# Performance work log

Measured on AMD Instinct MI355X. Metric: run time of the kernel, lower is better.

Reference implementation:

```python
import jax, jax.numpy as jnp
import numpy as np

EMBED = 1024
HEADS = 16
HEAD_DIM = EMBED // HEADS


def setup_inputs() -> dict:
    key = jax.random.key(0)
    ks = jax.random.split(key, 10)
    B, S = 2, 2048
    x = jax.random.normal(ks[0], (B, S, EMBED), dtype=jnp.float32)
    s = 1.0 / np.sqrt(EMBED)
    Wq = jax.random.normal(ks[1], (EMBED, EMBED), dtype=jnp.float32) * s
    Wk = jax.random.normal(ks[2], (EMBED, EMBED), dtype=jnp.float32) * s
    Wv = jax.random.normal(ks[3], (EMBED, EMBED), dtype=jnp.float32) * s
    Wo = jax.random.normal(ks[4], (EMBED, EMBED), dtype=jnp.float32) * s
    bq = jnp.zeros((EMBED,), jnp.float32)
    bk = jnp.zeros((EMBED,), jnp.float32)
    bv = jnp.zeros((EMBED,), jnp.float32)
    bo = jnp.zeros((EMBED,), jnp.float32)
    J = jax.random.normal(ks[5], (HEADS, HEAD_DIM, HEAD_DIM), dtype=jnp.float32) * 0.02
    lam = jnp.asarray(0.5, jnp.float32)
    return {"x": x, "Wq": Wq, "bq": bq, "Wk": Wk, "bk": bk,
            "Wv": Wv, "bv": bv, "Wo": Wo, "bo": bo, "J": J, "lam": lam}


def reference(x, Wq, bq, Wk, bk, Wv, bv, Wo, bo, J, lam):
    B, S, E = x.shape
    H, hd = HEADS, HEAD_DIM
    scale = np.sqrt(hd).astype(np.float32)

    def split_heads(t):  # (B,S,E) -> (B,H,S,hd)
        return t.reshape(B, S, H, hd).transpose(0, 2, 1, 3)

    Q = split_heads(x @ Wq + bq)
    K = split_heads(x @ Wk + bk)
    V = split_heads(x @ Wv + bv)

    scores = jnp.einsum('bhid,bhjd->bhij', Q, K) / scale
    Qn = jnp.tanh(Q)
    Kn = jnp.tanh(K)
    # bilinear correction: tanh(Q) J tanh(K)^T per head
    delta = jnp.einsum('bhid,hde,bhje->bhij', Qn, J, Kn)
    scores = scores + lam * delta

    causal = jnp.triu(jnp.ones((S, S), dtype=bool), k=1)  # True above diagonal
    scores = jnp.where(causal[None, None], -jnp.inf, scores)

    probs = jax.nn.softmax(scores, axis=-1)
    out = jnp.einsum('bhij,bhjd->bhid', probs, V)
    out = out.transpose(0, 2, 1, 3).reshape(B, S, E)
    return out @ Wo + bo
```

## Files before the change

### kernel.cpp

```cpp
#include <hip/hip_runtime.h>
#include <cstdint>
#include <cstddef>

typedef __bf16 bf16x8 __attribute__((ext_vector_type(8)));
typedef short  s16x8  __attribute__((ext_vector_type(8)));
typedef float  f32x4  __attribute__((ext_vector_type(4)));
typedef unsigned int u32x4 __attribute__((ext_vector_type(4)));

#define MFMA16(a, b, c) __builtin_amdgcn_mfma_f32_16x16x32_bf16((a), (b), (c), 0, 0, 0)

typedef __attribute__((address_space(3))) unsigned int       lds_uint;
typedef const __attribute__((address_space(1))) unsigned int glb_uint;

static __device__ __forceinline__ void gload_lds16(const void* g, void* l) {
  __builtin_amdgcn_global_load_lds((glb_uint*)g, (lds_uint*)l, 16, 0, 0);
}

static __device__ __forceinline__ unsigned short f2bf(float f) {
  unsigned u = __builtin_bit_cast(unsigned, f);
  unsigned r = u + 0x7FFFu + ((u >> 16) & 1u);
  return (unsigned short)(r >> 16);
}
static __device__ __forceinline__ float bf2f(unsigned short u) {
  unsigned x = ((unsigned)u) << 16;
  return __builtin_bit_cast(float, x);
}
static __device__ __forceinline__ float fast_tanh(float x) {
  float e = __expf(2.f * x);
  return 1.f - 2.f / (e + 1.f);
}
static __device__ __forceinline__ unsigned cvt_pk_bf16(float lo, float hi) {
  unsigned r;
  asm("v_cvt_pk_bf16_f32 %0, %1, %2" : "=v"(r) : "v"(lo), "v"(hi));
  return r;
}

__global__ void k_f32_to_bf16(const float* __restrict__ src,
                              unsigned short* __restrict__ dst, int n4) {
  int i = blockIdx.x * blockDim.x + threadIdx.x;
  if (i >= n4) return;
  float4 v = reinterpret_cast<const float4*>(src)[i];
  ushort4 o;
  o.x = f2bf(v.x); o.y = f2bf(v.y); o.z = f2bf(v.z); o.w = f2bf(v.w);
  reinterpret_cast<ushort4*>(dst)[i] = o;
}

__global__ void k_transpose4_to_bf16(const float* __restrict__ s0,
                                     const float* __restrict__ s1,
                                     const float* __restrict__ s2,
                                     const float* __restrict__ s3,
                                     unsigned short* __restrict__ dstBase) {
  __shared__ float t[32][33];
  const int z = blockIdx.z;
  const float* src = (z == 0) ? s0 : (z == 1) ? s1 : (z == 2) ? s2 : s3;
  unsigned short* dst = dstBase + (size_t)z * 1048576;
  int c0 = blockIdx.x * 32, r0 = blockIdx.y * 32;
  int tx = threadIdx.x, ty = threadIdx.y;
#pragma unroll
  for (int i = 0; i < 4; ++i)
    t[ty + i * 8][tx] = src[(size_t)(r0 + ty + i * 8) * 1024 + c0 + tx];
  __syncthreads();
#pragma unroll
  for (int i = 0; i < 4; ++i)
    dst[(size_t)(c0 + ty + i * 8) * 1024 + r0 + tx] = f2bf(t[tx][ty + i * 8]);
}

template <int MODE>
__global__ __launch_bounds__(256) void k_gemm(
    const unsigned short* __restrict__ A, const unsigned short* __restrict__ Bt,
    int M, int N, int K,
    float* __restrict__ Cout, const float* __restrict__ bias) {
  __shared__ __align__(16) unsigned short Al[128 * 64];
  __shared__ __align__(16) unsigned short Bl[128 * 64];
  const int tid = threadIdx.x;
  const int lane = tid & 63, w = tid >> 6;
  const int wm = w >> 1, wn = w & 1;
  const int l15 = lane & 15, l4 = lane >> 4;
  const int m0 = blockIdx.y * 128, n0 = blockIdx.x * 128;

  const int srow = lane >> 3;
  const int schunk = (lane & 7) ^ srow;
  const unsigned short* Ag = A + (size_t)(m0 + (w << 5) + srow) * K + (schunk << 3);
  const unsigned short* Bg = Bt + (size_t)(n0 + (w << 5) + srow) * K + (schunk << 3);
  unsigned short* Alw = Al + (w << 5) * 64;
  unsigned short* Blw = Bl + (w << 5) * 64;

  const f32x4 zero4 = {0.f, 0.f, 0.f, 0.f};
  f32x4 acc[4][4];
#pragma unroll
  for (int i = 0; i < 4; ++i)
#pragma unroll
    for (int j = 0; j < 4; ++j) acc[i][j] = zero4;

  for (int k0 = 0; k0 < K; k0 += 64) {
#pragma unroll
    for (int p = 0; p < 4; ++p) {
      gload_lds16(Ag + (size_t)(p * 8) * K + k0, Alw + p * 8 * 64);
      gload_lds16(Bg + (size_t)(p * 8) * K + k0, Blw + p * 8 * 64);
    }
    __syncthreads();
#pragma unroll
    for (int c = 0; c < 2; ++c) {
      bf16x8 af[4], bfr[4];
#pragma unroll
      for (int i = 0; i < 4; ++i) {
        int ra = wm * 64 + i * 16 + l15;
        af[i] = *reinterpret_cast<const bf16x8*>(
            reinterpret_cast<const char*>(Al) + ra * 128 +
            ((c * 64 + l4 * 16) ^ ((ra & 7) << 4)));
        int rb = wn * 64 + i * 16 + l15;
        bfr[i] = *reinterpret_cast<const bf16x8*>(
            reinterpret_cast<const char*>(Bl) + rb * 128 +
            ((c * 64 + l4 * 16) ^ ((rb & 7) << 4)));
      }
#pragma unroll
      for (int i = 0; i < 4; ++i)
#pragma unroll
        for (int j = 0; j < 4; ++j) acc[i][j] = MFMA16(af[i], bfr[j], acc[i][j]);
    }
    __syncthreads();
  }

#pragma unroll
  for (int i = 0; i < 4; ++i)
#pragma unroll
    for (int j = 0; j < 4; ++j)
#pragma unroll
      for (int r = 0; r < 4; ++r) {
        int mrow = m0 + wm * 64 + i * 16 + l4 * 4 + r;
        int ncol = n0 + wn * 64 + j * 16 + l15;
        Cout[(size_t)mrow * N + ncol] = acc[i][j][r] + bias[ncol];
      }
}

__global__ __launch_bounds__(512, 2) void k_gemm256_qkv(
    const unsigned short* __restrict__ A, const unsigned short* __restrict__ Bt,
    int M, int N, int K,
    const float* __restrict__ bq, const float* __restrict__ bk,
    const float* __restrict__ bv,
    unsigned short* __restrict__ Qa, unsigned short* __restrict__ Ka,
    unsigned short* __restrict__ Vt, unsigned short* __restrict__ Qn) {
  __shared__ __align__(16) unsigned short Al[2][256 * 64];
  __shared__ __align__(16) unsigned short Bl[2][256 * 64];
  const int tid = threadIdx.x;
  const int lane = tid & 63;
  const int w = tid >> 6, wm = w >> 2, wn = w & 3;
  const int l15 = lane & 15, l4 = lane >> 4;
  const int nbx = N >> 8;
  const int bid = (int)blockIdx.x;
  const int lin = (bid & 7) * ((int)gridDim.x >> 3) + (bid >> 3);
  const int m0 = (lin / nbx) << 8, n0 = (lin % nbx) << 8;
  const int NT = K >> 6;

  const int strow = tid >> 3, stchunk = tid & 7;
  const int schunk = stchunk ^ (strow & 7);

  auto stage = [&](int slot, int kt, int hh) {
    const unsigned short* src = (hh < 2) ? A : Bt;
    const int base0 = (hh < 2) ? m0 : n0;
    unsigned short* dst = (hh < 2) ? &Al[slot][0] : &Bl[slot][0];
    const int hrow = (hh & 1) * 128;
#pragma unroll
    for (int i = 0; i < 2; ++i) {
      int row = hrow + i * 64 + strow;
      gload_lds16(src + (size_t)(base0 + row) * K + kt * 64 + schunk * 8,
                  dst + row * 64 + stchunk * 8);
    }
  };

  const f32x4 zero4 = {0.f, 0.f, 0.f, 0.f};
  f32x4 acc[8][4];
#pragma unroll
  for (int i = 0; i < 8; ++i)
#pragma unroll
    for (int j = 0; j < 4; ++j) acc[i][j] = zero4;

  stage(0, 0, 0); stage(0, 0, 1); stage(0, 0, 2); stage(0, 0, 3);
  stage(1, 1, 0); stage(1, 1, 1); stage(1, 1, 2); stage(1, 1, 3);
  asm volatile("s_waitcnt vmcnt(8)" ::: "memory");
  __builtin_amdgcn_s_barrier();

  bf16x8 af[4][2], bf0[2][2], bf1[2][2];

  for (int kt = 0; kt < NT; ++kt) {
    const int s = kt & 1;
    const char* As = (const char*)&Al[s][0];
    const char* Bs = (const char*)&Bl[s][0];
    const int kp2 = (kt + 2 < NT) ? kt + 2 : NT - 1;

#pragma unroll
    for (int i = 0; i < 4; ++i) {
      const int ra = wm * 128 + i * 16 + l15;
#pragma unroll
      for (int kk = 0; kk < 2; ++kk)
        af[i][kk] = *(const bf16x8*)(As + ra * 128 + (((kk * 4 + l4) ^ (ra & 7)) << 4));
    }
#pragma unroll
    for (int j = 0; j < 2; ++j) {
      const int rb = wn * 64 + j * 16 + l15;
#pragma unroll
      for (int kk = 0; kk < 2; ++kk)
        bf0[j][kk] = *(const bf16x8*)(Bs + rb * 128 + (((kk * 4 + l4) ^ (rb & 7)) << 4));
    }
    __builtin_amdgcn_s_barrier();
    asm volatile("s_waitcnt lgkmcnt(0)" ::: "memory");
    __builtin_amdgcn_sched_barrier(0);
    __builtin_amdgcn_s_setprio(1);
#pragma unroll
    for (int i = 0; i < 4; ++i)
#pragma unroll
      for (int j = 0; j < 2; ++j)
#pragma unroll
        for (int kk = 0; kk < 2; ++kk)
          acc[i][j] = MFMA16(af[i][kk], bf0[j][kk], acc[i][j]);
    __builtin_amdgcn_s_setprio(0);
    __builtin_amdgcn_s_barrier();

#pragma unroll
    for (int j = 0; j < 2; ++j) {
      const int rb = wn * 64 + (2 + j) * 16 + l15;
#pragma unroll
      for (int kk = 0; kk < 2; ++kk)
        bf1[j][kk] = *(const bf16x8*)(Bs + rb * 128 + (((kk * 4 + l4) ^ (rb & 7)) << 4));
    }
    __builtin_amdgcn_s_barrier();
    asm volatile("s_waitcnt lgkmcnt(0)" ::: "memory");
    __builtin_amdgcn_sched_barrier(0);
    __builtin_amdgcn_s_setprio(1);
#pragma unroll
    for (int i = 0; i < 4; ++i)
#pragma unroll
      for (int j = 0; j < 2; ++j)
#pragma unroll
        for (int kk = 0; kk < 2; ++kk)
          acc[i][2 + j] = MFMA16(af[i][kk], bf1[j][kk], acc[i][2 + j]);
    __builtin_amdgcn_s_setprio(0);
    __builtin_amdgcn_s_barrier();

#pragma unroll
    for (int i = 0; i < 4; ++i) {
      const int ra = wm * 128 + (4 + i) * 16 + l15;
#pragma unroll
      for (int kk = 0; kk < 2; ++kk)
        af[i][kk] = *(const bf16x8*)(As + ra * 128 + (((kk * 4 + l4) ^ (ra & 7)) << 4));
    }
    __builtin_amdgcn_s_barrier();
    asm volatile("s_waitcnt lgkmcnt(0)" ::: "memory");
    __builtin_amdgcn_sched_barrier(0);
    __builtin_amdgcn_s_setprio(1);
#pragma unroll
    for (int i = 0; i < 4; ++i)
#pragma unroll
      for (int j = 0; j < 2; ++j)
#pragma unroll
        for (int kk = 0; kk < 2; ++kk)
          acc[4 + i][2 + j] = MFMA16(af[i][kk], bf1[j][kk], acc[4 + i][2 + j]);
    __builtin_amdgcn_s_setprio(0);
    __builtin_amdgcn_s_barrier();

    stage(s, kp2, 0); stage(s, kp2, 1); stage(s, kp2, 2); stage(s, kp2, 3);
    __builtin_amdgcn_sched_barrier(0);
    __builtin_amdgcn_s_setprio(1);
#pragma unroll
    for (int i = 0; i < 4; ++i)
#pragma unroll
      for (int j = 0; j < 2; ++j)
#pragma unroll
        for (int kk = 0; kk < 2; ++kk)
          acc[4 + i][j] = MFMA16(af[i][kk], bf0[j][kk], acc[4 + i][j]);
    __builtin_amdgcn_s_setprio(0);
    asm volatile("s_waitcnt vmcnt(8)" ::: "memory");
    __builtin_amdgcn_s_barrier();
  }
  asm volatile("s_waitcnt vmcnt(0)" ::: "memory");

#pragma unroll
  for (int mf = 0; mf < 8; ++mf) {
#pragma unroll
    for (int nf = 0; nf < 4; ++nf) {
#pragma unroll
      for (int r = 0; r < 4; ++r) {
        const int mrow = m0 + wm * 128 + mf * 16 + l4 * 4 + r;
        const int ncol = n0 + wn * 64 + nf * 16 + l15;
        const float v = acc[mf][nf][r];
        const int proj = ncol >> 10, nn = ncol & 1023;
        const int h = nn >> 6, d = nn & 63;
        const int b = mrow >> 11, sq = mrow & 2047;
        const size_t t64 = (size_t)(b * 16 + h) * 2048 + sq;
        if (proj == 0) {
          float q = v + bq[nn];
          Qa[t64 * 128 + d] = f2bf(q * 0.125f);
          Qn[t64 * 64 + d] = f2bf(fast_tanh(q));
        } else if (proj == 1) {
          float kk = v + bk[nn];
          Ka[t64 * 128 + d] = f2bf(kk);
          Ka[t64 * 128 + 64 + d] = f2bf(fast_tanh(kk));
        } else {
          Vt[((size_t)(b * 16 + h) * 64 + d) * 2048 + sq] = f2bf(v + bv[nn]);
        }
      }
    }
  }
}

__global__ __launch_bounds__(256) void k_qnj(const unsigned short* __restrict__ Qn,
                                             const float* __restrict__ J,
                                             const float* __restrict__ lamPtr,
                                             unsigned short* __restrict__ Qa) {
  __shared__ float Jl[64 * 64];
  __shared__ float Ql[64 * 64];
  int bid = blockIdx.x;
  int bh = bid >> 5, sblk = bid & 31;
  int h = bh & 15;
  int tid = threadIdx.x;
  float lam = lamPtr[0];
  const float4* Jh = reinterpret_cast<const float4*>(J + (size_t)h * 4096);
#pragma unroll
  for (int p = 0; p < 4; ++p)
    reinterpret_cast<float4*>(Jl)[p * 256 + tid] = Jh[p * 256 + tid];
  size_t tok0 = (size_t)bh * 2048 + sblk * 64;
#pragma unroll
  for (int p = 0; p < 2; ++p) {
    int idx = p * 256 + tid;
    s16x8 v = *reinterpret_cast<const s16x8*>(Qn + tok0 * 64 + idx * 8);
#pragma unroll
    for (int j = 0; j < 8; ++j) Ql[idx * 8 + j] = bf2f((unsigned short)v[j]);
  }
  __syncthreads();
  int e = tid & 63, wq = tid >> 6;
#pragma unroll 1
  for (int pass = 0; pass < 16; ++pass) {
    int tok = pass * 4 + wq;
    float a0 = 0.f, a1 = 0.f;
#pragma unroll
    for (int d = 0; d < 64; d += 2) {
      a0 += Ql[tok * 64 + d] * Jl[d * 64 + e];
      a1 += Ql[tok * 64 + d + 1] * Jl[(d + 1) * 64 + e];
    }
    Qa[(tok0 + tok) * 128 + 64 + e] = f2bf(lam * (a0 + a1));
  }
}

__global__ __launch_bounds__(256) void k_attn(const unsigned short* __restrict__ Qa,
                                              const unsigned short* __restrict__ Ka,
                                              const unsigned short* __restrict__ Vt,
                                              unsigned short* __restrict__ Ob) {
  constexpr int S = 2048;
  __shared__ __align__(16) unsigned short Klds[2][64 * 128];
  __shared__ __align__(16) unsigned short Vtl[2][64 * 64];

  const int blk = (int)blockIdx.x;
  const int xg = blk & 7, idx = blk >> 3;
  const int bh = xg * 4 + (idx & 3);
  const int qt = 31 - (idx >> 2);
  const int b = bh >> 4, h = bh & 15;
  const int tid = threadIdx.x;
  const int lane = tid & 63, w = tid >> 6;
  const int l15 = lane & 15, l4 = lane >> 4;
  const int q0 = qt * 64;
  const size_t bhS = (size_t)bh * S;
  const unsigned short* Kbase = Ka + bhS * 128;
  const unsigned short* Vbase = Vt + (size_t)bh * 64 * 2048;
  const f32x4 zero4 = {0.f, 0.f, 0.f, 0.f};

  const int rowbase = w * 16 + (lane >> 4);
  const int rb7 = rowbase & 7;
  const int cK0 = (lane & 15) ^ rb7;
  const int cK1 = cK0 ^ 4;
  const int vdvrow = w * 16 + (lane >> 3);
  const int cV = (lane & 7) ^ ((lane >> 3) & 7);

  bf16x8 qf[4];
  {
    int qrow = q0 + w * 16 + l15;
#pragma unroll
    for (int c = 0; c < 4; ++c)
      qf[c] = *reinterpret_cast<const bf16x8*>(Qa + (bhS + qrow) * 128 + c * 32 + l4 * 8);
  }

  f32x4 oacc[4];
  float m_ = -__builtin_inff(), lsum = 0.f;
#pragma unroll
  for (int v = 0; v < 4; ++v) oacc[v] = zero4;

  const int I0 = (l15 + 32 * (l4 & 1)) * 4;
  const int I1 = I0 + 64;
  const bool hi4 = (lane & 32) != 0;

#pragma unroll
  for (int p = 0; p < 4; ++p)
    gload_lds16(Kbase + (size_t)(rowbase + 4 * p) * 128 + ((p & 1) ? cK1 : cK0) * 8,
                &Klds[0][(w * 16 + p * 4) * 128]);
#pragma unroll
  for (int p = 0; p < 2; ++p)
    gload_lds16(Vbase + (size_t)(vdvrow + 8 * p) * 2048 + cV * 8,
                &Vtl[0][(w * 16 + p * 8) * 64]);
  __syncthreads();

  for (int kt = 0; kt <= qt; ++kt) {
    const int cur = kt & 1;
    const bool lastStep = (kt == qt);

    if (!lastStep) {
      const int base = (kt + 1) * 64;
      const int nxt = cur ^ 1;
#pragma unroll
      for (int p = 0; p < 4; ++p)
        gload_lds16(Kbase + (size_t)(base + rowbase + 4 * p) * 128 + ((p & 1) ? cK1 : cK0) * 8,
                    &Klds[nxt][(w * 16 + p * 4) * 128]);
#pragma unroll
      for (int p = 0; p < 2; ++p)
        gload_lds16(Vbase + (size_t)(vdvrow + 8 * p) * 2048 + base + cV * 8,
                    &Vtl[nxt][(w * 16 + p * 8) * 64]);
    }

    const char* Kl = reinterpret_cast<const char*>(Klds[cur]);
    f32x4 sc[4];
    __builtin_amdgcn_s_setprio(1);
#pragma unroll
    for (int fn = 0; fn < 4; ++fn) {
      sc[fn] = zero4;
      const int krow = fn * 16 + l15;
#pragma unroll
      for (int c = 0; c < 4; ++c) {
        bf16x8 kf = *reinterpret_cast<const bf16x8*>(
            Kl + krow * 256 + (((c * 4 + l4) ^ (krow & 7)) << 4));
        sc[fn] = MFMA16(kf, qf[c], sc[fn]);
      }
    }
    __builtin_amdgcn_s_setprio(0);

    if (lastStep) {
      const int qloc = w * 16 + l15;
#pragma unroll
      for (int fn = 0; fn < 4; ++fn)
#pragma unroll
        for (int r = 0; r < 4; ++r)
          if (fn * 16 + l4 * 4 + r > qloc) sc[fn][r] = -__builtin_inff();
    }

    float mx = sc[0][0];
#pragma unroll
    for (int fn = 0; fn < 4; ++fn)
#pragma unroll
      for (int r = 0; r < 4; ++r) mx = fmaxf(mx, sc[fn][r]);
    mx = fmaxf(mx, __shfl_xor(mx, 16));
    mx = fmaxf(mx, __shfl_xor(mx, 32));
    const float mn = fmaxf(m_, mx);
    const float al = __expf(m_ - mn);
    float p_[4][4];
    float rs = 0.f;
#pragma unroll
    for (int fn = 0; fn < 4; ++fn)
#pragma unroll
      for (int r = 0; r < 4; ++r) {
        float e = __expf(sc[fn][r] - mn);
        p_[fn][r] = e;
        rs += e;
      }
    rs += __shfl_xor(rs, 16);
    rs += __shfl_xor(rs, 32);
    lsum = lsum * al + rs;
    m_ = mn;

#pragma unroll
    for (int r = 0; r < 4; ++r) {
      float albc = __shfl(al, l4 * 4 + r);
#pragma unroll
      for (int v = 0; v < 4; ++v) oacc[v][r] *= albc;
    }

    unsigned cp[4][2];
#pragma unroll
    for (int fn = 0; fn < 4; ++fn) {
      cp[fn][0] = cvt_pk_bf16(p_[fn][0], p_[fn][1]);
      cp[fn][1] = cvt_pk_bf16(p_[fn][2], p_[fn][3]);
    }

    const char* Vl = reinterpret_cast<const char*>(Vtl[cur]);
#pragma unroll
    for (int c2 = 0; c2 < 2; ++c2) {
      unsigned a0 = __builtin_amdgcn_ds_bpermute(I0, (int)cp[c2 * 2][0]);
      unsigned b0 = __builtin_amdgcn_ds_bpermute(I0, (int)cp[c2 * 2 + 1][0]);
      unsigned a1 = __builtin_amdgcn_ds_bpermute(I0, (int)cp[c2 * 2][1]);
      unsigned b1 = __builtin_amdgcn_ds_bpermute(I0, (int)cp[c2 * 2 + 1][1]);
      unsigned a2 = __builtin_amdgcn_ds_bpermute(I1, (int)cp[c2 * 2][0]);
      unsigned b2 = __builtin_amdgcn_ds_bpermute(I1, (int)cp[c2 * 2 + 1][0]);
      unsigned a3 = __builtin_amdgcn_ds_bpermute(I1, (int)cp[c2 * 2][1]);
      unsigned b3 = __builtin_amdgcn_ds_bpermute(I1, (int)cp[c2 * 2 + 1][1]);
      u32x4 pw = {hi4 ? b0 : a0, hi4 ? b1 : a1, hi4 ? b2 : a2, hi4 ? b3 : a3};
      bf16x8 pa = __builtin_bit_cast(bf16x8, pw);
      __builtin_amdgcn_s_setprio(1);
#pragma unroll
      for (int v = 0; v < 4; ++v) {
        const int dvrow = v * 16 + l15;
        bf16x8 vf = *reinterpret_cast<const bf16x8*>(
            Vl + dvrow * 128 + (((c2 * 4 + l4) ^ (dvrow & 7)) << 4));
        oacc[v] = MFMA16(pa, vf, oacc[v]);
      }
      __builtin_amdgcn_s_setprio(0);
    }

    __syncthreads();
  }

  float lbc[4];
#pragma unroll
  for (int r = 0; r < 4; ++r) lbc[r] = __shfl(lsum, l4 * 4 + r);
#pragma unroll
  for (int v = 0; v < 4; ++v) {
#pragma unroll
    for (int r = 0; r < 4; ++r) {
      int row = q0 + w * 16 + l4 * 4 + r;
      float o = oacc[v][r] / lbc[r];
      Ob[((size_t)b * S + row) * 1024 + h * 64 + v * 16 + l15] = f2bf(o);
    }
  }
}

extern "C" void kernel_launch(void* const* d_in, const int* in_sizes, int n_in,
                              void* d_out, int out_size, void* d_ws, size_t ws_size,
                              hipStream_t stream) {
  const float* x   = (const float*)d_in[0];
  const float* Wq  = (const float*)d_in[1];
  const float* bq  = (const float*)d_in[2];
  const float* Wk  = (const float*)d_in[3];
  const float* bk  = (const float*)d_in[4];
  const float* Wv  = (const float*)d_in[5];
  const float* bv  = (const float*)d_in[6];
  const float* Wo  = (const float*)d_in[7];
  const float* bo  = (const float*)d_in[8];
  const float* J   = (const float*)d_in[9];
  const float* lam = (const float*)d_in[10];
  float* out = (float*)d_out;

  char* ws = (char*)d_ws;
  unsigned short* xb     = (unsigned short*)(ws);
  unsigned short* Wt_qkv = (unsigned short*)(ws + 8388608);
  unsigned short* Wt_o   = (unsigned short*)(ws + 14680064);
  unsigned short* Qa     = (unsigned short*)(ws + 16777216);
  unsigned short* Ka     = (unsigned short*)(ws + 33554432);
  unsigned short* Vt     = (unsigned short*)(ws + 50331648);
  unsigned short* Qn     = (unsigned short*)(ws + 58720256);
  unsigned short* Ob     = (unsigned short*)(ws + 67108864);

  k_f32_to_bf16<<<4096, 256, 0, stream>>>(x, xb, 1048576);

  k_transpose4_to_bf16<<<dim3(32, 32, 4), dim3(32, 8), 0, stream>>>(
      Wq, Wk, Wv, Wo, Wt_qkv);

  k_gemm256_qkv<<<192, 512, 0, stream>>>(xb, Wt_qkv, 4096, 3072, 1024,
      bq, bk, bv, Qa, Ka, Vt, Qn);

  k_qnj<<<1024, 256, 0, stream>>>(Qn, J, lam, Qa);

  k_attn<<<1024, 256, 0, stream>>>(Qa, Ka, Vt, Ob);

  k_gemm<0><<<dim3(8, 32), 256, 0, stream>>>(Ob, Wt_o, 4096, 1024, 1024,
      out, bo);
}
```

Baseline: 195.4 us.

## Stage QKV GEMM tiles through registers instead of direct global-to-LDS loads

```diff
diff --git a/kernel.cpp b/kernel.cpp
--- a/kernel.cpp
+++ b/kernel.cpp
@@ -153,18 +153,25 @@
   const int NT = K >> 6;
 
   const int strow = tid >> 3, stchunk = tid & 7;
-  const int schunk = stchunk ^ (strow & 7);
-
-  auto stage = [&](int slot, int kt, int hh) {
-    const unsigned short* src = (hh < 2) ? A : Bt;
-    const int base0 = (hh < 2) ? m0 : n0;
-    unsigned short* dst = (hh < 2) ? &Al[slot][0] : &Bl[slot][0];
-    const int hrow = (hh & 1) * 128;
-#pragma unroll
-    for (int i = 0; i < 2; ++i) {
-      int row = hrow + i * 64 + strow;
-      gload_lds16(src + (size_t)(base0 + row) * K + kt * 64 + schunk * 8,
-                  dst + row * 64 + stchunk * 8);
+  const int swz = (stchunk ^ (strow & 7)) << 4;
+  const unsigned short* Ag = A + (size_t)(m0 + strow) * K + stchunk * 8;
+  const unsigned short* Bg = Bt + (size_t)(n0 + strow) * K + stchunk * 8;
+
+  s16x8 ra[4], rb[4];
+  auto loadRegs = [&](int kt) {
+#pragma unroll
+    for (int p = 0; p < 4; ++p) {
+      ra[p] = *reinterpret_cast<const s16x8*>(Ag + (size_t)(p * 64) * K + kt * 64);
+      rb[p] = *reinterpret_cast<const s16x8*>(Bg + (size_t)(p * 64) * K + kt * 64);
+    }
+  };
+  auto writeRegs = [&](int slot) {
+    char* Ad = reinterpret_cast<char*>(&Al[slot][0]);
+    char* Bd = reinterpret_cast<char*>(&Bl[slot][0]);
+#pragma unroll
+    for (int p = 0; p < 4; ++p) {
+      *reinterpret_cast<s16x8*>(Ad + (p * 64 + strow) * 128 + swz) = ra[p];
+      *reinterpret_cast<s16x8*>(Bd + (p * 64 + strow) * 128 + swz) = rb[p];
     }
   };
 
@@ -175,9 +182,10 @@
 #pragma unroll
     for (int j = 0; j < 4; ++j) acc[i][j] = zero4;
 
-  stage(0, 0, 0); stage(0, 0, 1); stage(0, 0, 2); stage(0, 0, 3);
-  stage(1, 1, 0); stage(1, 1, 1); stage(1, 1, 2); stage(1, 1, 3);
-  asm volatile("s_waitcnt vmcnt(8)" ::: "memory");
+  loadRegs(0);
+  writeRegs(0);
+  loadRegs(1 < NT ? 1 : 0);
+  asm volatile("s_waitcnt lgkmcnt(0)" ::: "memory");
   __builtin_amdgcn_s_barrier();
 
   bf16x8 af[4][2], bf0[2][2], bf1[2][2];
@@ -190,17 +198,17 @@
 
 #pragma unroll
     for (int i = 0; i < 4; ++i) {
-      const int ra = wm * 128 + i * 16 + l15;
+      const int ra_ = wm * 128 + i * 16 + l15;
 #pragma unroll
       for (int kk = 0; kk < 2; ++kk)
-        af[i][kk] = *(const bf16x8*)(As + ra * 128 + (((kk * 4 + l4) ^ (ra & 7)) << 4));
+        af[i][kk] = *(const bf16x8*)(As + ra_ * 128 + (((kk * 4 + l4) ^ (ra_ & 7)) << 4));
     }
 #pragma unroll
     for (int j = 0; j < 2; ++j) {
-      const int rb = wn * 64 + j * 16 + l15;
+      const int rb_ = wn * 64 + j * 16 + l15;
 #pragma unroll
       for (int kk = 0; kk < 2; ++kk)
-        bf0[j][kk] = *(const bf16x8*)(Bs + rb * 128 + (((kk * 4 + l4) ^ (rb & 7)) << 4));
+        bf0[j][kk] = *(const bf16x8*)(Bs + rb_ * 128 + (((kk * 4 + l4) ^ (rb_ & 7)) << 4));
     }
     __builtin_amdgcn_s_barrier();
     asm volatile("s_waitcnt lgkmcnt(0)" ::: "memory");
@@ -218,11 +226,12 @@
 
 #pragma unroll
     for (int j = 0; j < 2; ++j) {
-      const int rb = wn * 64 + (2 + j) * 16 + l15;
+      const int rb_ = wn * 64 + (2 + j) * 16 + l15;
 #pragma unroll
       for (int kk = 0; kk < 2; ++kk)
-        bf1[j][kk] = *(const bf16x8*)(Bs + rb * 128 + (((kk * 4 + l4) ^ (rb & 7)) << 4));
-    }
+        bf1[j][kk] = *(const bf16x8*)(Bs + rb_ * 128 + (((kk * 4 + l4) ^ (rb_ & 7)) << 4));
+    }
+    writeRegs(s ^ 1);
     __builtin_amdgcn_s_barrier();
     asm volatile("s_waitcnt lgkmcnt(0)" ::: "memory");
     __builtin_amdgcn_sched_barrier(0);
@@ -239,11 +248,12 @@
 
 #pragma unroll
     for (int i = 0; i < 4; ++i) {
-      const int ra = wm * 128 + (4 + i) * 16 + l15;
+      const int ra_ = wm * 128 + (4 + i) * 16 + l15;
 #pragma unroll
       for (int kk = 0; kk < 2; ++kk)
-        af[i][kk] = *(const bf16x8*)(As + ra * 128 + (((kk * 4 + l4) ^ (ra & 7)) << 4));
-    }
+        af[i][kk] = *(const bf16x8*)(As + ra_ * 128 + (((kk * 4 + l4) ^ (ra_ & 7)) << 4));
+    }
+    loadRegs(kp2);
     __builtin_amdgcn_s_barrier();
     asm volatile("s_waitcnt lgkmcnt(0)" ::: "memory");
     __builtin_amdgcn_sched_barrier(0);
@@ -258,8 +268,6 @@
     __builtin_amdgcn_s_setprio(0);
     __builtin_amdgcn_s_barrier();
 
-    stage(s, kp2, 0); stage(s, kp2, 1); stage(s, kp2, 2); stage(s, kp2, 3);
-    __builtin_amdgcn_sched_barrier(0);
     __builtin_amdgcn_s_setprio(1);
 #pragma unroll
     for (int i = 0; i < 4; ++i)
@@ -269,10 +277,8 @@
         for (int kk = 0; kk < 2; ++kk)
           acc[4 + i][j] = MFMA16(af[i][kk], bf0[j][kk], acc[4 + i][j]);
     __builtin_amdgcn_s_setprio(0);
-    asm volatile("s_waitcnt vmcnt(8)" ::: "memory");
-    __builtin_amdgcn_s_barrier();
-  }
-  asm volatile("s_waitcnt vmcnt(0)" ::: "memory");
+    __builtin_amdgcn_s_barrier();
+  }
 
 #pragma unroll
   for (int mf = 0; mf < 8; ++mf) {
```

Result: no change. 197.9 us (+1.3%).
